# Kernel tuning notes

Hardware: AMD Instinct MI355X
Metric: run time of the kernel (lower is better)

The kernel has to match this reference:

```python
import jax, jax.numpy as jnp
import numpy as np

N, E, D_IN, D, HEADS = 8192, 2048, 256, 256, 4
EPS = 1e-5
NEG = -1e9  # large negative instead of -inf (rows guaranteed non-empty anyway)


def _layernorm(x, g, b):
    mu = jnp.mean(x, axis=-1, keepdims=True)
    var = jnp.mean(jnp.square(x - mu), axis=-1, keepdims=True)
    return (x - mu) * jax.lax.rsqrt(var + EPS) * g + b


def _mha(q_x, kv_x, in_w, in_b, out_w, out_b, mask):
    """torch nn.MultiheadAttention (batch=1, eval) with boolean attn_mask.
    q_x: [Lq, D], kv_x: [Lk, D], mask: [Lq, Lk] True = blocked."""
    hd = D // HEADS
    wq, wk, wv = jnp.split(in_w, 3, axis=0)   # each [D, D]
    bq, bk, bv = jnp.split(in_b, 3, axis=0)
    q = (q_x @ wq.T + bq).reshape(-1, HEADS, hd).transpose(1, 0, 2)  # [h, Lq, hd]
    k = (kv_x @ wk.T + bk).reshape(-1, HEADS, hd).transpose(1, 0, 2)
    v = (kv_x @ wv.T + bv).reshape(-1, HEADS, hd).transpose(1, 0, 2)
    scores = jnp.einsum('hqd,hkd->hqk', q, k) / jnp.sqrt(jnp.asarray(hd, q.dtype))
    scores = jnp.where(mask[None, :, :], NEG, scores)
    attn = jax.nn.softmax(scores, axis=-1)
    out = jnp.einsum('hqk,hkd->hqd', attn, v)           # [h, Lq, hd]
    out = out.transpose(1, 0, 2).reshape(-1, D)          # [Lq, D]
    return out @ out_w.T + out_b


def setup_inputs() -> dict:
    key = jax.random.key(0)
    ks = jax.random.split(key, 12)
    s = 0.02
    x_0 = jax.random.normal(ks[0], (N, D_IN), jnp.float32)
    x_1 = jax.random.normal(ks[1], (E, D_IN), jnp.float32)
    H = (jax.random.uniform(ks[2], (N, E)) < 0.01).astype(jnp.float32)
    H = H.at[jnp.arange(N), jnp.arange(N) % E].set(1.0)
    return {
        'x_0': x_0, 'x_1': x_1, 'incidence_1': H,
        'node_w': jax.random.normal(ks[3], (D, D_IN), jnp.float32) * s,
        'node_b': jnp.zeros((D,), jnp.float32),
        'edge_w': jax.random.normal(ks[4], (D, D_IN), jnp.float32) * s,
        'edge_b': jnp.zeros((D,), jnp.float32),
        'n2e_in_w': jax.random.normal(ks[5], (3 * D, D), jnp.float32) * s,
        'n2e_in_b': jnp.zeros((3 * D,), jnp.float32),
        'n2e_out_w': jax.random.normal(ks[6], (D, D), jnp.float32) * s,
        'n2e_out_b': jnp.zeros((D,), jnp.float32),
        'e2n_in_w': jax.random.normal(ks[7], (3 * D, D), jnp.float32) * s,
        'e2n_in_b': jnp.zeros((3 * D,), jnp.float32),
        'e2n_out_w': jax.random.normal(ks[8], (D, D), jnp.float32) * s,
        'e2n_out_b': jnp.zeros((D,), jnp.float32),
        'norm1_g': jnp.ones((D,), jnp.float32),
        'norm1_b': jnp.zeros((D,), jnp.float32),
        'norm2_g': jnp.ones((D,), jnp.float32),
        'norm2_b': jnp.zeros((D,), jnp.float32),
    }


def reference(x_0, x_1, incidence_1, node_w, node_b, edge_w, edge_b,
              n2e_in_w, n2e_in_b, n2e_out_w, n2e_out_b,
              e2n_in_w, e2n_in_b, e2n_out_w, e2n_out_b,
              norm1_g, norm1_b, norm2_g, norm2_b):
    H = incidence_1                      # [N, E]
    x_0_p = x_0 @ node_w.T + node_b      # [N, D]
    x_1_p = x_1 @ edge_w.T + edge_b      # [E, D]
    # node -> edge: edges query nodes, mask where H.T == 0
    x_1_u = _mha(x_1_p, x_0_p, n2e_in_w, n2e_in_b, n2e_out_w, n2e_out_b,
                 H.T == 0)
    x_1_u = _layernorm(x_1_p + x_1_u, norm1_g, norm1_b)
    # edge -> node: nodes query updated edges, mask where H == 0
    x_0_u = _mha(x_0_p, x_1_u, e2n_in_w, e2n_in_b, e2n_out_w, e2n_out_b,
                 H == 0)
    x_0_u = _layernorm(x_0_p + x_0_u, norm2_g, norm2_b)
    return (x_0_u, x_1_u)
```

## Files before the change

kernel.cpp:

```cpp
#include <hip/hip_runtime.h>
#include <hip/hip_bf16.h>

using bf16 = __hip_bfloat16;
typedef __attribute__((ext_vector_type(4))) float  f32x4;
typedef __attribute__((ext_vector_type(8))) short  s16x8;

#define QSTRIDE 1040
#define ASTRIDE 520
#define BSTRIDE 2064
#define CMAX 256
#define RMAX 128

struct ConvDesc { const float* src[14]; int dstoff[14]; int cnt[14]; };

__global__ __launch_bounds__(256)
void conv_weights(ConvDesc d, bf16* __restrict__ dst, int* __restrict__ cz, int czn)
{
    const int seg = blockIdx.x >> 6;
    const int blk = blockIdx.x & 63;
    if (seg == 14) {
        for (int i = blk * 256 + threadIdx.x; i < czn; i += 64 * 256)
            cz[i] = 0;
        return;
    }
    const float* __restrict__ s = d.src[seg];
    bf16* __restrict__ o = dst + d.dstoff[seg];
    const int n = d.cnt[seg];
    for (int i = blk * 256 + threadIdx.x; i < n; i += 64 * 256)
        o[i] = __float2bfloat16(s[i]);
}

__global__ __launch_bounds__(256)
void build_lists(const float* __restrict__ H, int* __restrict__ col_cnt,
                 unsigned short* __restrict__ col_idx, int* __restrict__ row_cnt,
                 unsigned short* __restrict__ row_idx)
{
    const int wv   = threadIdx.x >> 6;
    const int lane = threadIdx.x & 63;
    const int n    = blockIdx.x * 4 + wv;
    const float* __restrict__ Hp = H + (size_t)n * 2048;
    unsigned short* __restrict__ rl = row_idx + (size_t)n * RMAX;

    const unsigned long long below = (lane == 63) ? ~0ull >> 1
                                    : ((1ull << lane) - 1);

    int base = 0;
#pragma unroll 4
    for (int c = 0; c < 32; c++) {
        const float v = Hp[c * 64 + lane];
        const bool nz = (v != 0.f);
        const unsigned long long mask = __ballot(nz);
        if (nz) {
            const int e = c * 64 + lane;
            const int pos = base + __popcll(mask & below);
            if (pos < RMAX) rl[pos] = (unsigned short)e;
            const int sc = atomicAdd(&col_cnt[e], 1);
            if (sc < CMAX) col_idx[(size_t)e * CMAX + sc] = (unsigned short)n;
        }
        base += __popcll(mask);
    }
    if (lane == 0) row_cnt[n] = (base < RMAX) ? base : RMAX;
}

__global__ __launch_bounds__(256, 2)
void gemm_proj(const float* __restrict__ X0, const float* __restrict__ X1,
               const bf16* __restrict__ Wc, const bf16* __restrict__ biasc,
               bf16* __restrict__ outB)
{
    __shared__ __align__(16) bf16 As[4 * QSTRIDE];
    __shared__ __align__(16) bf16 Bs[4 * QSTRIDE];

    const int t    = threadIdx.x;
    const int lane = t & 63;
    const int w    = t >> 6;
    const int wm   = (w >> 1) * 64;
    const int wn   = (w & 1) * 64;
    const int bt   = blockIdx.x >> 1;
    const int tn   = (blockIdx.x & 1) * 128;
    if (bt >= 80) return;

    const float* __restrict__ A = (bt < 64) ? X0 : X1;
    const int arow = (bt < 64) ? bt * 128 : (bt - 64) * 128;
    const bf16* __restrict__ W    = Wc    + ((bt < 64) ? 0 : 65536);
    const bf16* __restrict__ bias = biasc + ((bt < 64) ? 0 : 256);
    const int tm = bt * 128;

    f32x4 acc[4][4];
#pragma unroll
    for (int i = 0; i < 4; i++)
#pragma unroll
        for (int j = 0; j < 4; j++)
#pragma unroll
            for (int r = 0; r < 4; r++) acc[i][j][r] = 0.f;

    const int m0 = t >> 2,         q0 = t & 3;
    const int m1 = (t + 256) >> 2, q1 = (t + 256) & 3;
    const int fq = lane >> 4, fr = lane & 15;

    for (int k0 = 0; k0 < 256; k0 += 32) {
        f32x4 a0l = *(const f32x4*)(A + (size_t)(arow + m0) * 256 + k0 + q0 * 8);
        f32x4 a0h = *(const f32x4*)(A + (size_t)(arow + m0) * 256 + k0 + q0 * 8 + 4);
        f32x4 a1l = *(const f32x4*)(A + (size_t)(arow + m1) * 256 + k0 + q1 * 8);
        f32x4 a1h = *(const f32x4*)(A + (size_t)(arow + m1) * 256 + k0 + q1 * 8 + 4);
        union { s16x8 v; bf16 e[8]; } u0, u1;
#pragma unroll
        for (int j = 0; j < 4; j++) {
            u0.e[j] = __float2bfloat16(a0l[j]); u0.e[4 + j] = __float2bfloat16(a0h[j]);
            u1.e[j] = __float2bfloat16(a1l[j]); u1.e[4 + j] = __float2bfloat16(a1h[j]);
        }
        s16x8 sb0 = *(const s16x8*)(W + (size_t)(tn + m0) * 256 + k0 + q0 * 8);
        s16x8 sb1 = *(const s16x8*)(W + (size_t)(tn + m1) * 256 + k0 + q1 * 8);

        __syncthreads();
        *(s16x8*)&As[q0 * QSTRIDE + m0 * 8] = u0.v;
        *(s16x8*)&As[q1 * QSTRIDE + m1 * 8] = u1.v;
        *(s16x8*)&Bs[q0 * QSTRIDE + m0 * 8] = sb0;
        *(s16x8*)&Bs[q1 * QSTRIDE + m1 * 8] = sb1;
        __syncthreads();

        s16x8 af[4], bfv[4];
#pragma unroll
        for (int i = 0; i < 4; i++) {
            af[i]  = *(const s16x8*)&As[fq * QSTRIDE + (wm + i * 16 + fr) * 8];
            bfv[i] = *(const s16x8*)&Bs[fq * QSTRIDE + (wn + i * 16 + fr) * 8];
        }
#pragma unroll
        for (int i = 0; i < 4; i++)
#pragma unroll
            for (int j = 0; j < 4; j++)
                acc[i][j] = __builtin_amdgcn_mfma_f32_16x16x32_bf16(
                    af[i], bfv[j], acc[i][j], 0, 0, 0);
    }

#pragma unroll
    for (int j = 0; j < 4; j++) {
        const int ncol = tn + wn + j * 16 + fr;
        const float bj = __bfloat162float(bias[ncol]);
#pragma unroll
        for (int i = 0; i < 4; i++)
#pragma unroll
            for (int r = 0; r < 4; r++) {
                const int mrow = tm + wm + i * 16 + fq * 4 + r;
                outB[(size_t)mrow * 256 + ncol] = __float2bfloat16(acc[i][j][r] + bj);
            }
    }
}

__global__ __launch_bounds__(256, 2)
void gemm_dual(const bf16* __restrict__ A0, const bf16* __restrict__ W0,
               const bf16* __restrict__ bias0, bf16* __restrict__ out0,
               int N0, int tiles0, int nblk0,
               const bf16* __restrict__ A1, const bf16* __restrict__ W1,
               const bf16* __restrict__ bias1, bf16* __restrict__ out1,
               int N1, int tiles1)
{
    __shared__ __align__(16) bf16 As[4 * QSTRIDE];
    __shared__ __align__(16) bf16 Bs[4 * QSTRIDE];

    const int t    = threadIdx.x;
    const int lane = t & 63;
    const int w    = t >> 6;
    const int wm   = (w >> 1) * 64;
    const int wn   = (w & 1) * 64;

    const bool second = (blockIdx.x >= (unsigned)nblk0);
    const int  bi     = second ? (blockIdx.x - nblk0) : blockIdx.x;
    const bf16* __restrict__ A    = second ? A1 : A0;
    const bf16* __restrict__ W    = second ? W1 : W0;
    const bf16* __restrict__ bias = second ? bias1 : bias0;
    bf16* __restrict__ outB       = second ? out1 : out0;
    const int N      = second ? N1 : N0;
    const int tilesN = second ? tiles1 : tiles0;
    const int tm = (bi / tilesN) * 128;
    const int tn = (bi % tilesN) * 128;

    f32x4 acc[4][4];
#pragma unroll
    for (int i = 0; i < 4; i++)
#pragma unroll
        for (int j = 0; j < 4; j++)
#pragma unroll
            for (int r = 0; r < 4; r++) acc[i][j][r] = 0.f;

    const int m0 = t >> 2,         q0 = t & 3;
    const int m1 = (t + 256) >> 2, q1 = (t + 256) & 3;
    const int fq = lane >> 4, fr = lane & 15;

    for (int k0 = 0; k0 < 256; k0 += 32) {
        s16x8 sa0 = *(const s16x8*)(A + (size_t)(tm + m0) * 256 + k0 + q0 * 8);
        s16x8 sa1 = *(const s16x8*)(A + (size_t)(tm + m1) * 256 + k0 + q1 * 8);
        s16x8 sb0 = *(const s16x8*)(W + (size_t)(tn + m0) * 256 + k0 + q0 * 8);
        s16x8 sb1 = *(const s16x8*)(W + (size_t)(tn + m1) * 256 + k0 + q1 * 8);

        __syncthreads();
        *(s16x8*)&As[q0 * QSTRIDE + m0 * 8] = sa0;
        *(s16x8*)&As[q1 * QSTRIDE + m1 * 8] = sa1;
        *(s16x8*)&Bs[q0 * QSTRIDE + m0 * 8] = sb0;
        *(s16x8*)&Bs[q1 * QSTRIDE + m1 * 8] = sb1;
        __syncthreads();

        s16x8 af[4], bfv[4];
#pragma unroll
        for (int i = 0; i < 4; i++) {
            af[i]  = *(const s16x8*)&As[fq * QSTRIDE + (wm + i * 16 + fr) * 8];
            bfv[i] = *(const s16x8*)&Bs[fq * QSTRIDE + (wn + i * 16 + fr) * 8];
        }
#pragma unroll
        for (int i = 0; i < 4; i++)
#pragma unroll
            for (int j = 0; j < 4; j++)
                acc[i][j] = __builtin_amdgcn_mfma_f32_16x16x32_bf16(
                    af[i], bfv[j], acc[i][j], 0, 0, 0);
    }

#pragma unroll
    for (int j = 0; j < 4; j++) {
        const int ncol = tn + wn + j * 16 + fr;
        const float bj = __bfloat162float(bias[ncol]);
#pragma unroll
        for (int i = 0; i < 4; i++)
#pragma unroll
            for (int r = 0; r < 4; r++) {
                const int mrow = tm + wm + i * 16 + fq * 4 + r;
                outB[(size_t)mrow * N + ncol] = __float2bfloat16(acc[i][j][r] + bj);
            }
    }
}

__global__ __launch_bounds__(256, 2)
void gemm_ln(const bf16* __restrict__ A, const bf16* __restrict__ W,
             const float* __restrict__ biasF, const bf16* __restrict__ xp,
             const float* __restrict__ g, const float* __restrict__ b,
             float* __restrict__ outF, bf16* __restrict__ outB)
{
    __shared__ __align__(16) bf16 As[4 * ASTRIDE];
    __shared__ __align__(16) bf16 Bs[4 * BSTRIDE];
    __shared__ float rs1[64], rs2[64];

    const int t    = threadIdx.x;
    const int lane = t & 63;
    const int w    = t >> 6;
    const int fq   = lane >> 4;
    const int fr   = lane & 15;
    const int tm   = blockIdx.x * 64;

    if (t < 64) { rs1[t] = 0.f; rs2[t] = 0.f; }

    f32x4 acc[4][4];
#pragma unroll
    for (int i = 0; i < 4; i++)
#pragma unroll
        for (int j = 0; j < 4; j++)
#pragma unroll
            for (int r = 0; r < 4; r++) acc[i][j][r] = 0.f;

    const int mA = t >> 2, qA = t & 3;

    for (int k0 = 0; k0 < 256; k0 += 32) {
        s16x8 sa = *(const s16x8*)(A + (size_t)(tm + mA) * 256 + k0 + qA * 8);
        s16x8 sb[4];
#pragma unroll
        for (int s = 0; s < 4; s++)
            sb[s] = *(const s16x8*)(W + (size_t)(mA + 64 * s) * 256 + k0 + qA * 8);

        __syncthreads();
        *(s16x8*)&As[qA * ASTRIDE + mA * 8] = sa;
#pragma unroll
        for (int s = 0; s < 4; s++)
            *(s16x8*)&Bs[qA * BSTRIDE + (mA + 64 * s) * 8] = sb[s];
        __syncthreads();

        s16x8 af[4], bfv[4];
#pragma unroll
        for (int i = 0; i < 4; i++) {
            af[i]  = *(const s16x8*)&As[fq * ASTRIDE + (i * 16 + fr) * 8];
            bfv[i] = *(const s16x8*)&Bs[fq * BSTRIDE + (w * 64 + i * 16 + fr) * 8];
        }
#pragma unroll
        for (int i = 0; i < 4; i++)
#pragma unroll
            for (int j = 0; j < 4; j++)
                acc[i][j] = __builtin_amdgcn_mfma_f32_16x16x32_bf16(
                    af[i], bfv[j], acc[i][j], 0, 0, 0);
    }

    float bj[4], gj[4], bbj[4];
    int colv[4];
#pragma unroll
    for (int j = 0; j < 4; j++) {
        colv[j] = w * 64 + j * 16 + fr;
        bj[j]  = biasF[colv[j]];
        gj[j]  = g[colv[j]];
        bbj[j] = b[colv[j]];
    }

#pragma unroll
    for (int i = 0; i < 4; i++) {
#pragma unroll
        for (int r = 0; r < 4; r++) {
            const int row = i * 16 + fq * 4 + r;
            float t1 = 0.f, t2 = 0.f;
#pragma unroll
            for (int j = 0; j < 4; j++) {
                float v = acc[i][j][r] + bj[j]
                        + __bfloat162float(xp[(size_t)(tm + row) * 256 + colv[j]]);
                acc[i][j][r] = v;
                t1 += v;
                t2 += v * v;
            }
#pragma unroll
            for (int o = 1; o < 16; o <<= 1) {
                t1 += __shfl_xor(t1, o);
                t2 += __shfl_xor(t2, o);
            }
            if (fr == 0) {
                atomicAdd(&rs1[row], t1);
                atomicAdd(&rs2[row], t2);
            }
        }
    }
    __syncthreads();

#pragma unroll
    for (int i = 0; i < 4; i++) {
#pragma unroll
        for (int r = 0; r < 4; r++) {
            const int row = i * 16 + fq * 4 + r;
            const float mu  = rs1[row] * (1.f / 256.f);
            const float var = rs2[row] * (1.f / 256.f) - mu * mu;
            const float rstd = rsqrtf(var + 1e-5f);
#pragma unroll
            for (int j = 0; j < 4; j++) {
                const float y = (acc[i][j][r] - mu) * rstd * gj[j] + bbj[j];
                outF[(size_t)(tm + row) * 256 + colv[j]] = y;
                if (outB) outB[(size_t)(tm + row) * 256 + colv[j]] = __float2bfloat16(y);
            }
        }
    }
}

__global__ __launch_bounds__(256)
void sparse_attn(const bf16* __restrict__ Q, int qs,
                 const bf16* __restrict__ Kb, const bf16* __restrict__ Vb, int kvs,
                 const int* __restrict__ cnts, const unsigned short* __restrict__ idx,
                 int lmax, int idxmask, bf16* __restrict__ out)
{
    __shared__ float sc[4][CMAX];
    __shared__ unsigned short nls[CMAX];
    const int qi   = blockIdx.x;
    const int h    = threadIdx.x >> 6;
    const int lane = threadIdx.x & 63;
    const int grp  = lane >> 3;
    const int sub  = lane & 7;

    int n = cnts[qi];
    if (n > lmax) n = lmax;

    if (h == 0)
        for (int i = lane; i < n; i += 64)
            nls[i] = (unsigned short)(((int)idx[(size_t)qi * lmax + i]) & idxmask);
    __syncthreads();

    if (n <= 0) {
        out[(size_t)qi * 256 + h * 64 + lane] = __float2bfloat16(0.f);
        return;
    }

    float qv[8];
    {
        union { f32x4 v; unsigned short u[8]; } qu;
        qu.v = *(const f32x4*)(Q + (size_t)qi * qs + h * 64 + sub * 8);
#pragma unroll
        for (int j = 0; j < 8; j++)
            qv[j] = __uint_as_float(((unsigned)qu.u[j]) << 16) * 0.125f;
    }

    float mx = -1e30f;
#pragma unroll 2
    for (int base = 0; base < n; base += 8) {
        const int i = base + grp;
        float s = -1e30f;
        if (i < n) {
            const int nb = nls[i];
            union { f32x4 v; unsigned short u[8]; } ku;
            ku.v = *(const f32x4*)(Kb + (size_t)nb * kvs + h * 64 + sub * 8);
            float a = 0.f;
#pragma unroll
            for (int j = 0; j < 8; j++)
                a += __uint_as_float(((unsigned)ku.u[j]) << 16) * qv[j];
            a += __shfl_xor(a, 1);
            a += __shfl_xor(a, 2);
            a += __shfl_xor(a, 4);
            if (sub == 0) sc[h][i] = a;
            s = a;
        }
        mx = fmaxf(mx, s);
    }
#pragma unroll
    for (int o = 32; o > 0; o >>= 1) mx = fmaxf(mx, __shfl_xor(mx, o));

    float sum = 0.f;
    for (int base = 0; base < n; base += 64) {
        const int i = base + lane;
        if (i < n) {
            const float p = __expf(sc[h][i] - mx);
            sc[h][i] = p;
            sum += p;
        }
    }
#pragma unroll
    for (int o = 32; o > 0; o >>= 1) sum += __shfl_xor(sum, o);
    const float inv = 1.f / sum;

    float oa[8];
#pragma unroll
    for (int j = 0; j < 8; j++) oa[j] = 0.f;
#pragma unroll 2
    for (int base = 0; base < n; base += 8) {
        const int i = base + grp;
        if (i < n) {
            const float p = sc[h][i];
            const int nb = nls[i];
            union { f32x4 v; unsigned short u[8]; } vu;
            vu.v = *(const f32x4*)(Vb + (size_t)nb * kvs + h * 64 + sub * 8);
#pragma unroll
            for (int j = 0; j < 8; j++)
                oa[j] += p * __uint_as_float(((unsigned)vu.u[j]) << 16);
        }
    }
#pragma unroll
    for (int j = 0; j < 8; j++) {
        oa[j] += __shfl_xor(oa[j], 8);
        oa[j] += __shfl_xor(oa[j], 16);
        oa[j] += __shfl_xor(oa[j], 32);
    }
    if (grp == 0) {
        union { s16x8 v; bf16 e[8]; } ou;
#pragma unroll
        for (int j = 0; j < 8; j++) ou.e[j] = __float2bfloat16(oa[j] * inv);
        *(s16x8*)(out + (size_t)qi * 256 + h * 64 + sub * 8) = ou.v;
    }
}

extern "C" void kernel_launch(void* const* d_in, const int* in_sizes, int n_in,
                              void* d_out, int out_size, void* d_ws, size_t ws_size,
                              hipStream_t stream)
{
    const int N = 8192, E = 2048;

    float* out0 = (float*)d_out;
    float* out1 = (float*)d_out + (size_t)N * 256;

    char* wp = (char*)d_ws;
    auto carve = [&](size_t bytes) { void* p = wp; wp += (bytes + 15) & ~size_t(15); return p; };

    bf16*  wcat    = (bf16*)          carve(657408 * 2);
    int*   col_cnt = (int*)           carve((size_t)E * 4);
    int*   row_cnt = (int*)           carve((size_t)N * 4);
    unsigned short* col_idx = (unsigned short*)carve((size_t)E * CMAX * 2);
    unsigned short* row_idx = (unsigned short*)carve((size_t)N * RMAX * 2);
    bf16*  xp01    = (bf16*) carve((size_t)(N + E) * 256 * 2);
    bf16*  kvq     = (bf16*) carve((size_t)N * 768 * 2);
    bf16*  q1      = (bf16*) carve((size_t)E * 256 * 2);
    bf16*  attn1   = (bf16*) carve((size_t)E * 256 * 2);
    bf16*  x1u_b   = (bf16*) carve((size_t)E * 256 * 2);
    bf16*  kv2     = (bf16*) carve((size_t)E * 512 * 2);
    bf16*  attn2   = (bf16*) carve((size_t)N * 256 * 2);

    bf16* x0p = xp01;
    bf16* x1p = xp01 + (size_t)N * 256;

    const int O_PW   = 0;
    const int O_PB   = 131072;
    const int O_KVQ  = 131584;
    const int O_KVQB = 328192;
    const int O_Q1W  = 328960;
    const int O_Q1B  = 394496;
    const int O_KV2W = 394752;
    const int O_KV2B = 525824;
    const int O_O1W  = 526336;
    const int O_O2W  = 591872;

    ConvDesc cd;
    const float* srcs[14] = {
        (const float*)d_in[3], (const float*)d_in[5],
        (const float*)d_in[4], (const float*)d_in[6],
        (const float*)d_in[7] + 65536, (const float*)d_in[11],
        (const float*)d_in[8] + 256,   (const float*)d_in[12],
        (const float*)d_in[7],         (const float*)d_in[8],
        (const float*)d_in[11] + 65536,(const float*)d_in[12] + 256,
        (const float*)d_in[9],         (const float*)d_in[13]
    };
    const int offs[14] = {O_PW, O_PW + 65536, O_PB, O_PB + 256,
                          O_KVQ, O_KVQ + 131072, O_KVQB, O_KVQB + 512,
                          O_Q1W, O_Q1B, O_KV2W, O_KV2B, O_O1W, O_O2W};
    const int cnts[14] = {65536, 65536, 256, 256, 131072, 65536, 512, 256,
                          65536, 256, 131072, 512, 65536, 65536};
    for (int i = 0; i < 14; i++) { cd.src[i] = srcs[i]; cd.dstoff[i] = offs[i]; cd.cnt[i] = cnts[i]; }

    conv_weights<<<15 * 64, 256, 0, stream>>>(cd, wcat, col_cnt, E);

    build_lists<<<2048, 256, 0, stream>>>((const float*)d_in[2], col_cnt, col_idx,
                                          row_cnt, row_idx);

    gemm_proj<<<160, 256, 0, stream>>>((const float*)d_in[0], (const float*)d_in[1],
                                       wcat + O_PW, wcat + O_PB, xp01);

    gemm_dual<<<384 + 32, 256, 0, stream>>>(x0p, wcat + O_KVQ, wcat + O_KVQB, kvq,
                                            768, 6, 384,
                                            x1p, wcat + O_Q1W, wcat + O_Q1B, q1,
                                            256, 2);

    sparse_attn<<<E, 256, 0, stream>>>(q1, 256, kvq, kvq + 256, 768,
                                       col_cnt, col_idx, CMAX, N - 1, attn1);
    gemm_ln<<<E / 64, 256, 0, stream>>>(attn1, wcat + O_O1W, (const float*)d_in[10],
                                        x1p, (const float*)d_in[15], (const float*)d_in[16],
                                        out1, x1u_b);

    gemm_dual<<<64, 256, 0, stream>>>(x1u_b, wcat + O_KV2W, wcat + O_KV2B, kv2,
                                      512, 4, 64,
                                      nullptr, nullptr, nullptr, nullptr, 256, 2);
    sparse_attn<<<N, 256, 0, stream>>>(kvq + 512, 768, kv2, kv2 + 256, 512,
                                       row_cnt, row_idx, RMAX, E - 1, attn2);
    gemm_ln<<<N / 64, 256, 0, stream>>>(attn2, wcat + O_O2W, (const float*)d_in[14],
                                        x0p, (const float*)d_in[17], (const float*)d_in[18],
                                        out0, nullptr);
}
```

Measured before the change: 312.3 us.

## Tile incidence scan and aggregate column counts in shared memory before global atomics

The incidence-list build now gives each block a 256-row by 64-column tile instead of four full rows. Column hits are staged per column in shared memory and appended to the global column list with one atomic per column per block. This replaces the per-nonzero global atomics on the column counters. Row counts are now built with atomics too, so the zeroing kernel also clears the row counters, which assumes they sit right after the column counters in memory. Row list order becomes nondeterministic, row counts are no longer clamped, and a column with more than 24 hits in one tile would silently lose entries.

```diff
diff --git a/kernel.cpp b/kernel.cpp
--- a/kernel.cpp
+++ b/kernel.cpp
@@ -10,6 +10,7 @@
 #define BSTRIDE 2064
 #define CMAX 256
 #define RMAX 128
+#define STG  24
 
 struct ConvDesc { const float* src[14]; int dstoff[14]; int cnt[14]; };
 
@@ -35,31 +36,52 @@
                  unsigned short* __restrict__ col_idx, int* __restrict__ row_cnt,
                  unsigned short* __restrict__ row_idx)
 {
+    __shared__ int lcnt[64];
+    __shared__ unsigned short stage[64][STG];
+
     const int wv   = threadIdx.x >> 6;
     const int lane = threadIdx.x & 63;
-    const int n    = blockIdx.x * 4 + wv;
-    const float* __restrict__ Hp = H + (size_t)n * 2048;
-    unsigned short* __restrict__ rl = row_idx + (size_t)n * RMAX;
-
-    const unsigned long long below = (lane == 63) ? ~0ull >> 1
-                                    : ((1ull << lane) - 1);
-
-    int base = 0;
+    const int r0   = (blockIdx.x >> 5) * 256;
+    const int c0   = (blockIdx.x & 31) * 64;
+
+    if (threadIdx.x < 64) lcnt[threadIdx.x] = 0;
+    __syncthreads();
+
+    const unsigned long long below = (1ull << lane) - 1;
+
 #pragma unroll 4
-    for (int c = 0; c < 32; c++) {
-        const float v = Hp[c * 64 + lane];
+    for (int it = 0; it < 64; it++) {
+        const int r = r0 + wv * 64 + it;
+        const float v = H[(size_t)r * 2048 + c0 + lane];
         const bool nz = (v != 0.f);
         const unsigned long long mask = __ballot(nz);
+        const int cnt = __popcll(mask);
+        int base = 0;
+        if (lane == 0 && cnt) base = atomicAdd(&row_cnt[r], cnt);
+        base = __shfl(base, 0);
         if (nz) {
-            const int e = c * 64 + lane;
             const int pos = base + __popcll(mask & below);
-            if (pos < RMAX) rl[pos] = (unsigned short)e;
-            const int sc = atomicAdd(&col_cnt[e], 1);
-            if (sc < CMAX) col_idx[(size_t)e * CMAX + sc] = (unsigned short)n;
-        }
-        base += __popcll(mask);
-    }
-    if (lane == 0) row_cnt[n] = (base < RMAX) ? base : RMAX;
+            if (pos < RMAX)
+                row_idx[(size_t)r * RMAX + pos] = (unsigned short)(c0 + lane);
+            const int lp = atomicAdd(&lcnt[lane], 1);
+            if (lp < STG) stage[lane][lp] = (unsigned short)r;
+        }
+    }
+    __syncthreads();
+
+    if (threadIdx.x < 64) {
+        const int c = c0 + threadIdx.x;
+        int cnt = lcnt[threadIdx.x];
+        if (cnt > STG) cnt = STG;
+        if (cnt) {
+            const int base = atomicAdd(&col_cnt[c], cnt);
+            for (int i = 0; i < cnt; i++) {
+                const int pos = base + i;
+                if (pos < CMAX)
+                    col_idx[(size_t)c * CMAX + pos] = stage[threadIdx.x][i];
+            }
+        }
+    }
 }
 
 __global__ __launch_bounds__(256, 2)
@@ -498,9 +520,9 @@
                           65536, 256, 131072, 512, 65536, 65536};
     for (int i = 0; i < 14; i++) { cd.src[i] = srcs[i]; cd.dstoff[i] = offs[i]; cd.cnt[i] = cnts[i]; }
 
-    conv_weights<<<15 * 64, 256, 0, stream>>>(cd, wcat, col_cnt, E);
-
-    build_lists<<<2048, 256, 0, stream>>>((const float*)d_in[2], col_cnt, col_idx,
+    conv_weights<<<15 * 64, 256, 0, stream>>>(cd, wcat, col_cnt, E + N);
+
+    build_lists<<<1024, 256, 0, stream>>>((const float*)d_in[2], col_cnt, col_idx,
                                           row_cnt, row_idx);
 
     gemm_proj<<<160, 256, 0, stream>>>((const float*)d_in[0], (const float*)d_in[1],
```

Result: faster. 299.3 us (-4.1%).

## Replace atomic column-list build with row bitmaps and a column scan kernel

Applied to the files above, without the earlier changes.

The row pass now reads each incidence row with vectorized f32x4 loads and stores a 2048-bit bitmap per node alongside its row list. A new build_cols kernel rebuilds each edge's node list by scanning all 8192 bitmap rows, one column per lane. This removes the global atomicAdd traffic and the zeroing of col_cnt, and it makes the column lists deterministic and sorted. The cost is that build_cols runs only 32 single-wave blocks, each doing a serial 8192-step dependent scan, so that stage is latency-bound and may be slow. It also needs an extra 2 MB bitmap buffer.

```diff
diff --git a/kernel.cpp b/kernel.cpp
--- a/kernel.cpp
+++ b/kernel.cpp
@@ -14,15 +14,10 @@
 struct ConvDesc { const float* src[14]; int dstoff[14]; int cnt[14]; };
 
 __global__ __launch_bounds__(256)
-void conv_weights(ConvDesc d, bf16* __restrict__ dst, int* __restrict__ cz, int czn)
+void conv_weights(ConvDesc d, bf16* __restrict__ dst)
 {
     const int seg = blockIdx.x >> 6;
     const int blk = blockIdx.x & 63;
-    if (seg == 14) {
-        for (int i = blk * 256 + threadIdx.x; i < czn; i += 64 * 256)
-            cz[i] = 0;
-        return;
-    }
     const float* __restrict__ s = d.src[seg];
     bf16* __restrict__ o = dst + d.dstoff[seg];
     const int n = d.cnt[seg];
@@ -31,9 +26,8 @@
 }
 
 __global__ __launch_bounds__(256)
-void build_lists(const float* __restrict__ H, int* __restrict__ col_cnt,
-                 unsigned short* __restrict__ col_idx, int* __restrict__ row_cnt,
-                 unsigned short* __restrict__ row_idx)
+void build_rows(const float* __restrict__ H, unsigned long long* __restrict__ bmp,
+                int* __restrict__ row_cnt, unsigned short* __restrict__ row_idx)
 {
     const int wv   = threadIdx.x >> 6;
     const int lane = threadIdx.x & 63;
@@ -41,25 +35,58 @@
     const float* __restrict__ Hp = H + (size_t)n * 2048;
     unsigned short* __restrict__ rl = row_idx + (size_t)n * RMAX;
 
-    const unsigned long long below = (lane == 63) ? ~0ull >> 1
-                                    : ((1ull << lane) - 1);
-
+    const unsigned long long below = (1ull << lane) - 1;
+
+    f32x4 v[8];
+#pragma unroll
+    for (int g = 0; g < 8; g++)
+        v[g] = *(const f32x4*)(Hp + g * 256 + lane * 4);
+
+    unsigned long long mw = 0;
     int base = 0;
-#pragma unroll 4
-    for (int c = 0; c < 32; c++) {
-        const float v = Hp[c * 64 + lane];
-        const bool nz = (v != 0.f);
-        const unsigned long long mask = __ballot(nz);
-        if (nz) {
-            const int e = c * 64 + lane;
-            const int pos = base + __popcll(mask & below);
-            if (pos < RMAX) rl[pos] = (unsigned short)e;
-            const int sc = atomicAdd(&col_cnt[e], 1);
-            if (sc < CMAX) col_idx[(size_t)e * CMAX + sc] = (unsigned short)n;
-        }
-        base += __popcll(mask);
-    }
+#pragma unroll
+    for (int g = 0; g < 8; g++) {
+#pragma unroll
+        for (int sub = 0; sub < 4; sub++) {
+            const bool nz = (v[g][sub] != 0.f);
+            const unsigned long long mask = __ballot(nz);
+            if (nz) {
+                const int pos = base + __popcll(mask & below);
+                if (pos < RMAX)
+                    rl[pos] = (unsigned short)(g * 256 + lane * 4 + sub);
+            }
+            base += __popcll(mask);
+            if (lane == g * 4 + sub) mw = mask;
+        }
+    }
+    if (lane < 32) bmp[(size_t)n * 32 + lane] = mw;
     if (lane == 0) row_cnt[n] = (base < RMAX) ? base : RMAX;
+}
+
+__global__ __launch_bounds__(64)
+void build_cols(const unsigned long long* __restrict__ bmp,
+                int* __restrict__ col_cnt, unsigned short* __restrict__ col_idx)
+{
+    const int widx = blockIdx.x;
+    const int lane = threadIdx.x;
+    const int c    = (widx >> 2) * 256 + lane * 4 + (widx & 3);
+    unsigned short* __restrict__ cl = col_idx + (size_t)c * CMAX;
+
+    int cnt = 0;
+    for (int r0 = 0; r0 < 8192; r0 += 8) {
+        unsigned long long w[8];
+#pragma unroll
+        for (int k = 0; k < 8; k++)
+            w[k] = bmp[(size_t)(r0 + k) * 32 + widx];
+#pragma unroll
+        for (int k = 0; k < 8; k++) {
+            if ((w[k] >> lane) & 1ull) {
+                if (cnt < CMAX) cl[cnt] = (unsigned short)(r0 + k);
+                cnt++;
+            }
+        }
+    }
+    col_cnt[c] = (cnt < CMAX) ? cnt : CMAX;
 }
 
 __global__ __launch_bounds__(256, 2)
@@ -459,6 +486,7 @@
     int*   row_cnt = (int*)           carve((size_t)N * 4);
     unsigned short* col_idx = (unsigned short*)carve((size_t)E * CMAX * 2);
     unsigned short* row_idx = (unsigned short*)carve((size_t)N * RMAX * 2);
+    unsigned long long* bmp = (unsigned long long*)carve((size_t)N * 32 * 8);
     bf16*  xp01    = (bf16*) carve((size_t)(N + E) * 256 * 2);
     bf16*  kvq     = (bf16*) carve((size_t)N * 768 * 2);
     bf16*  q1      = (bf16*) carve((size_t)E * 256 * 2);
@@ -498,10 +526,10 @@
                           65536, 256, 131072, 512, 65536, 65536};
     for (int i = 0; i < 14; i++) { cd.src[i] = srcs[i]; cd.dstoff[i] = offs[i]; cd.cnt[i] = cnts[i]; }
 
-    conv_weights<<<15 * 64, 256, 0, stream>>>(cd, wcat, col_cnt, E);
-
-    build_lists<<<2048, 256, 0, stream>>>((const float*)d_in[2], col_cnt, col_idx,
-                                          row_cnt, row_idx);
+    conv_weights<<<14 * 64, 256, 0, stream>>>(cd, wcat);
+
+    build_rows<<<2048, 256, 0, stream>>>((const float*)d_in[2], bmp, row_cnt, row_idx);
+    build_cols<<<32, 64, 0, stream>>>(bmp, col_cnt, col_idx);
 
     gemm_proj<<<160, 256, 0, stream>>>((const float*)d_in[0], (const float*)d_in[1],
                                        wcat + O_PW, wcat + O_PB, xp01);
```

New measurement: 1.034 ms. +231.0%, slower.
